# Kernel optimization log

Measured on AMD Instinct MI355X. Metric: run time of the kernel, lower is better.

## Reference

```python
import jax, jax.numpy as jnp
import numpy as np

DIM = 4096

def _fwht_unnormalized(y):
    # y: (T, d), iterative radix-2 butterfly, unnormalized Sylvester WHT
    d = y.shape[-1]
    h = 1
    while h < d:
        y = y.reshape(-1, d // (2 * h), 2, h)
        a = y[..., 0, :]
        b = y[..., 1, :]
        y = jnp.stack([a + b, a - b], axis=-2).reshape(-1, d)
        h *= 2
    return y

def setup_inputs() -> dict:
    key = jax.random.key(0)
    x = jax.random.normal(key, (4, 2048, DIM), dtype=jnp.float32)
    return {"x": x}

def reference(x):
    # Original: x_flat @ H.T where H is built recursively with a 1/sqrt(n)
    # division at EVERY recursion level. H is symmetric, and equals the
    # unnormalized Sylvester Hadamard times 2^{-L(L+1)/4}, L = log2(d).
    shape = x.shape
    d = shape[-1]
    L = int(round(np.log2(d)))
    scale = np.float32(2.0 ** (-(L * (L + 1)) / 4.0))
    y = _fwht_unnormalized(x.reshape(-1, d))
    return (y * scale).reshape(shape)
```

## Files before the change

kernel.cpp:

```cpp
#include <hip/hip_runtime.h>


constexpr int DIM = 4096;
constexpr int PITCH = 68;

__global__ __launch_bounds__(64) void fwht4096_kernel(const float* __restrict__ x,
                                                      float* __restrict__ y) {
    __shared__ float buf[64 * PITCH];
    const int lane = threadIdx.x;
    const long long row = blockIdx.x;

    float v[64];

    {
        const float4* src = reinterpret_cast<const float4*>(x + row * DIM + lane * 64);
#pragma unroll
        for (int q = 0; q < 16; ++q) {
            float4 t = src[q];
            v[4 * q + 0] = t.x;
            v[4 * q + 1] = t.y;
            v[4 * q + 2] = t.z;
            v[4 * q + 3] = t.w;
        }
    }

#pragma unroll
    for (int h = 1; h < 64; h <<= 1) {
#pragma unroll
        for (int i = 0; i < 64; i += 2 * h) {
#pragma unroll
            for (int k = 0; k < h; ++k) {
                float a = v[i + k];
                float b = v[i + k + h];
                v[i + k]     = a + b;
                v[i + k + h] = a - b;
            }
        }
    }

    {
        float* wp = buf + lane * PITCH;
#pragma unroll
        for (int q = 0; q < 16; ++q) {
            float4 t;
            t.x = v[4 * q + 0];
            t.y = v[4 * q + 1];
            t.z = v[4 * q + 2];
            t.w = v[4 * q + 3];
            reinterpret_cast<float4*>(wp)[q] = t;
        }
    }
    __syncthreads();

#pragma unroll
    for (int m = 0; m < 64; ++m) {
        v[m] = buf[m * PITCH + lane];
    }

#pragma unroll
    for (int h = 1; h < 64; h <<= 1) {
#pragma unroll
        for (int i = 0; i < 64; i += 2 * h) {
#pragma unroll
            for (int k = 0; k < h; ++k) {
                float a = v[i + k];
                float b = v[i + k + h];
                v[i + k]     = a + b;
                v[i + k + h] = a - b;
            }
        }
    }

    const float scale = 0x1p-39f;
    float* dst = y + row * DIM + lane;
#pragma unroll
    for (int m = 0; m < 64; ++m) {
        dst[m * 64] = v[m] * scale;
    }
}

extern "C" void kernel_launch(void* const* d_in, const int* in_sizes, int n_in,
                              void* d_out, int out_size, void* d_ws, size_t ws_size,
                              hipStream_t stream) {
    const float* x = (const float*)d_in[0];
    float* y = (float*)d_out;
    const int nrows = in_sizes[0] / DIM;
    fwht4096_kernel<<<nrows, 64, 0, stream>>>(x, y);
}
```

Measured before the change: 229.5 us.

## Halve shared transpose buffer with two-phase exchange and nontemporal stores

The 64x64 transpose through shared memory now runs in two halves, so the LDS buffer holds only 32 rows and each block uses half as much shared memory. Launch bounds request 4 waves per SIMD to push occupancy up. Output stores use nontemporal hints to bypass cache retention. In exchange there are extra barriers, and a second 64-float register array raises register pressure, which may cause spills under the tighter bound.

```diff
diff --git a/kernel.cpp b/kernel.cpp
--- a/kernel.cpp
+++ b/kernel.cpp
@@ -4,9 +4,9 @@
 constexpr int DIM = 4096;
 constexpr int PITCH = 68;
 
-__global__ __launch_bounds__(64) void fwht4096_kernel(const float* __restrict__ x,
-                                                      float* __restrict__ y) {
-    __shared__ float buf[64 * PITCH];
+__global__ __launch_bounds__(64, 4) void fwht4096_kernel(const float* __restrict__ x,
+                                                         float* __restrict__ y) {
+    __shared__ float buf[32 * PITCH];
     const int lane = threadIdx.x;
     const long long row = blockIdx.x;
 
@@ -38,23 +38,34 @@
         }
     }
 
-    {
+    float w[64];
+    if (lane < 32) {
         float* wp = buf + lane * PITCH;
 #pragma unroll
         for (int q = 0; q < 16; ++q) {
-            float4 t;
-            t.x = v[4 * q + 0];
-            t.y = v[4 * q + 1];
-            t.z = v[4 * q + 2];
-            t.w = v[4 * q + 3];
+            float4 t = make_float4(v[4 * q], v[4 * q + 1], v[4 * q + 2], v[4 * q + 3]);
             reinterpret_cast<float4*>(wp)[q] = t;
         }
     }
     __syncthreads();
+#pragma unroll
+    for (int m = 0; m < 32; ++m) {
+        w[m] = buf[m * PITCH + lane];
+    }
+    __syncthreads();
 
+    if (lane >= 32) {
+        float* wp = buf + (lane - 32) * PITCH;
 #pragma unroll
-    for (int m = 0; m < 64; ++m) {
-        v[m] = buf[m * PITCH + lane];
+        for (int q = 0; q < 16; ++q) {
+            float4 t = make_float4(v[4 * q], v[4 * q + 1], v[4 * q + 2], v[4 * q + 3]);
+            reinterpret_cast<float4*>(wp)[q] = t;
+        }
+    }
+    __syncthreads();
+#pragma unroll
+    for (int m = 0; m < 32; ++m) {
+        w[32 + m] = buf[m * PITCH + lane];
     }
 
 #pragma unroll
@@ -63,10 +74,10 @@
         for (int i = 0; i < 64; i += 2 * h) {
 #pragma unroll
             for (int k = 0; k < h; ++k) {
-                float a = v[i + k];
-                float b = v[i + k + h];
-                v[i + k]     = a + b;
-                v[i + k + h] = a - b;
+                float a = w[i + k];
+                float b = w[i + k + h];
+                w[i + k]     = a + b;
+                w[i + k + h] = a - b;
             }
         }
     }
@@ -75,7 +86,7 @@
     float* dst = y + row * DIM + lane;
 #pragma unroll
     for (int m = 0; m < 64; ++m) {
-        dst[m * 64] = v[m] * scale;
+        __builtin_nontemporal_store(w[m] * scale, dst + m * 64);
     }
 }
 
```

Result: no change. 233.3 us (+1.6%).
